# Optimization experiments

Measured on AMD Instinct MI355X. Metric: run time of the kernel, lower is better.

Reference implementation:

```python
import jax, jax.numpy as jnp
import numpy as np
import math

B, N, CS = 1, 2048, 384
H, C, PQK, PV = 12, 16, 4, 8
INF, EPS = 100000.0, 1e-08


def setup_inputs() -> dict:
    key = jax.random.key(0)
    ks = jax.random.split(key, 16)
    hc = H * C
    hpq = H * PQK * 3
    hpkv = H * (PQK + PV) * 3
    cod = H * (C + 4 * PV)
    sc = 0.02
    return {
        "s": jax.random.normal(ks[0], (B, N, CS), jnp.float32),
        "rot": jax.random.normal(ks[1], (B, N, 3, 3), jnp.float32),
        "trans": jax.random.normal(ks[2], (B, N, 3), jnp.float32),
        "mask": jnp.ones((B, N), jnp.float32),
        "Wq": jax.random.normal(ks[3], (hc, CS), jnp.float32) * sc,
        "bq": jnp.zeros((hc,), jnp.float32),
        "Wkv": jax.random.normal(ks[4], (2 * hc, CS), jnp.float32) * sc,
        "bkv": jnp.zeros((2 * hc,), jnp.float32),
        "Wqp": jax.random.normal(ks[5], (hpq, CS), jnp.float32) * sc,
        "bqp": jnp.zeros((hpq,), jnp.float32),
        "Wkvp": jax.random.normal(ks[6], (hpkv, CS), jnp.float32) * sc,
        "bkvp": jnp.zeros((hpkv,), jnp.float32),
        "head_weights": jnp.full((H,), 0.541324854612918, jnp.float32),
        "Wout": jax.random.normal(ks[7], (CS, H * cod // H), jnp.float32) * sc,
        "bout": jnp.zeros((CS,), jnp.float32),
    }


def _points(s, W, b, rot, trans, npts):
    # torch.split into 3 chunks of H*npts then stack at -1 -> [B,N,H*npts,3]
    p = jnp.einsum("bni,oi->bno", s, W) + b
    p = jnp.moveaxis(p.reshape(B, N, 3, H * npts), -2, -1)  # [B,N,H*npts,3]
    p = jnp.einsum("bnij,bnmj->bnmi", rot, p) + trans[:, :, None, :]  # rigid apply
    return p.reshape(B, N, H, npts, 3)


def reference(s, rot, trans, mask, Wq, bq, Wkv, bkv, Wqp, bqp, Wkvp, bkvp, head_weights, Wout, bout):
    q = (jnp.einsum("bni,oi->bno", s, Wq) + bq).reshape(B, N, H, C)
    kv = (jnp.einsum("bni,oi->bno", s, Wkv) + bkv).reshape(B, N, H, 2 * C)
    k, v = kv[..., :C], kv[..., C:]

    q_pts = _points(s, Wqp, bqp, rot, trans, PQK)             # [B,N,H,PQK,3]
    kv_pts = _points(s, Wkvp, bkvp, rot, trans, PQK + PV)
    k_pts, v_pts = kv_pts[..., :PQK, :], kv_pts[..., PQK:, :]  # [B,N,H,PQK,3], [B,N,H,PV,3]

    a = jnp.einsum("bihc,bjhc->bhij", q, k) * math.sqrt(1.0 / (3 * C))

    # sum_{p,c} |q_pts_i - k_pts_j|^2 via norm expansion (avoids [N,N,P,3])
    q2 = jnp.moveaxis(jnp.sum(q_pts ** 2, axis=(-1, -2)), -1, 1)  # [B,H,N]
    k2 = jnp.moveaxis(jnp.sum(k_pts ** 2, axis=(-1, -2)), -1, 1)
    cross = jnp.einsum("bihpc,bjhpc->bhij", q_pts, k_pts)
    d2 = q2[..., :, None] + k2[..., None, :] - 2.0 * cross       # [B,H,N,N]

    hw = jax.nn.softplus(head_weights) * math.sqrt(1.0 / (3 * (PQK * 9.0 / 2)))
    pt_att = -0.5 * hw[None, :, None, None] * d2

    sq_mask = INF * (mask[:, None, :, None] * mask[:, None, None, :] - 1.0)  # [B,1,N,N]
    a = jax.nn.softmax(a + pt_att + sq_mask, axis=-1)

    o = jnp.einsum("bhij,bjhc->bihc", a, v).reshape(B, N, H * C)
    o_pt = jnp.einsum("bhij,bjhpc->bihpc", a, v_pts)             # [B,N,H,PV,3]
    o_pt = jnp.einsum("bnji,bnhpj->bnhpi", rot, o_pt - trans[:, :, None, None, :])  # invert_apply

    dists = jnp.sqrt(jnp.sum(o_pt ** 2, axis=-1) + EPS).reshape(B, N, H * PV)
    o_pt_f = o_pt.reshape(B, N, H * PV, 3)
    feats = jnp.concatenate([o, o_pt_f[..., 0], o_pt_f[..., 1], o_pt_f[..., 2], dists], axis=-1)
    return jnp.einsum("bnf,of->bno", feats, Wout) + bout
```

## Files before the change

kernel.cpp:

```cpp
#include <hip/hip_runtime.h>
#include <hip/hip_bf16.h>
#include <cstdint>
#include <cstddef>

#define Hh    12
#define Nseq  2048
#define PSTR  1152
#define EPSm  1e-8f
#define MASKV 1024.0f

typedef unsigned short ushort_t;
typedef __attribute__((ext_vector_type(8))) short bf8_t;
typedef __attribute__((ext_vector_type(4))) short s4_t;
typedef __attribute__((ext_vector_type(4))) float f4_t;

#define OFF_PALL   0
#define OFF_WALLB  2359296
#define OFF_BALL   2580480
#define OFF_SB     2581632
#define OFF_WOUTB  2974848
#define OFF_FEATSB 3085440
#define OFF_AU     3675264
#define OFF_KU     4068480
#define OFF_VU     4461696
#define WS_FLOATS  5051520

__device__ __forceinline__ ushort_t bfr(float x) {
    union { float f; uint32_t u; } v; v.f = x;
    uint32_t r = v.u + 0x7FFFu + ((v.u >> 16) & 1u);
    return (ushort_t)(r >> 16);
}

__global__ __launch_bounds__(256) void prep(
    const float* __restrict__ s, const float* __restrict__ Wout,
    const float* __restrict__ Wq, const float* __restrict__ Wkv,
    const float* __restrict__ Wqp, const float* __restrict__ Wkvp,
    const float* __restrict__ bq, const float* __restrict__ bkv,
    const float* __restrict__ bqp, const float* __restrict__ bkvp,
    ushort_t* __restrict__ Wallb, float* __restrict__ ball,
    ushort_t* __restrict__ sb, ushort_t* __restrict__ Woutb)
{
    int idx = blockIdx.x * 256 + threadIdx.x;
    if (idx < 1152 * 384) {
        int r = idx / 384, c = idx % 384;
        float v;
        if (r < 192)      v = Wq [(size_t)r * 384 + c];
        else if (r < 576) v = Wkv[(size_t)(r - 192) * 384 + c];
        else if (r < 720) v = Wqp[(size_t)(r - 576) * 384 + c];
        else              v = Wkvp[(size_t)(r - 720) * 384 + c];
        Wallb[idx] = bfr(v);
    }
    if (idx < 1152) {
        float v;
        if (idx < 192)      v = bq[idx];
        else if (idx < 576) v = bkv[idx - 192];
        else if (idx < 720) v = bqp[idx - 576];
        else                v = bkvp[idx - 720];
        ball[idx] = v;
    }
    if (idx < 2048 * 384) sb[idx] = bfr(s[idx]);
    if (idx < 384 * 576)  Woutb[idx] = bfr(Wout[idx]);
}

template<int BM, int BN>
__global__ __launch_bounds__(256) void gemm_mfma(
    const ushort_t* __restrict__ A, const ushort_t* __restrict__ W,
    const float* __restrict__ bias, float* __restrict__ C,
    int M, int Nn, int K)
{
    constexpr int WM = BM / 2, WN = BN / 2;
    constexpr int MI = WM / 16, NJ = WN / 16;
    __shared__ ushort_t As[BM][40];
    __shared__ ushort_t Bs[BN][40];

    const int bm = blockIdx.y * BM;
    const int bn = blockIdx.x * BN;
    const int t  = threadIdx.x;
    const int w  = t >> 6, lane = t & 63;
    const int m  = lane & 15, quad = lane >> 4;
    const int wm = (w >> 1) * WM, wn = (w & 1) * WN;

    f4_t acc[MI][NJ];
    #pragma unroll
    for (int i2 = 0; i2 < MI; ++i2)
        #pragma unroll
        for (int j2 = 0; j2 < NJ; ++j2)
            acc[i2][j2] = (f4_t){0.f, 0.f, 0.f, 0.f};

    for (int k0 = 0; k0 < K; k0 += 32) {
        #pragma unroll
        for (int u = 0; u < BM / 64; ++u) {
            int e = t + u * 256;
            int r = e >> 2, kk = (e & 3) * 8;
            *(uint4*)&As[r][kk] = *(const uint4*)&A[(size_t)(bm + r) * K + k0 + kk];
        }
        #pragma unroll
        for (int u = 0; u < BN / 64; ++u) {
            int e = t + u * 256;
            int r = e >> 2, kk = (e & 3) * 8;
            *(uint4*)&Bs[r][kk] = *(const uint4*)&W[(size_t)(bn + r) * K + k0 + kk];
        }
        __syncthreads();
        bf8_t af[MI], bfv[NJ];
        #pragma unroll
        for (int x = 0; x < MI; ++x) af[x]  = *(const bf8_t*)&As[wm + x * 16 + m][quad * 8];
        #pragma unroll
        for (int x = 0; x < NJ; ++x) bfv[x] = *(const bf8_t*)&Bs[wn + x * 16 + m][quad * 8];
        #pragma unroll
        for (int i2 = 0; i2 < MI; ++i2)
            #pragma unroll
            for (int j2 = 0; j2 < NJ; ++j2)
                acc[i2][j2] = __builtin_amdgcn_mfma_f32_16x16x32_bf16(
                    af[i2], bfv[j2], acc[i2][j2], 0, 0, 0);
        __syncthreads();
    }

    #pragma unroll
    for (int j2 = 0; j2 < NJ; ++j2) {
        int col = bn + wn + j2 * 16 + m;
        float bb = bias[col];
        #pragma unroll
        for (int i2 = 0; i2 < MI; ++i2)
            #pragma unroll
            for (int r = 0; r < 4; ++r) {
                int row = bm + wm + i2 * 16 + quad * 4 + r;
                C[(size_t)row * Nn + col] = acc[i2][j2][r] + bb;
            }
    }
}

__global__ __launch_bounds__(128) void pack_aug(
    const float* __restrict__ Pall, const float* __restrict__ rot,
    const float* __restrict__ trans, const float* __restrict__ mask,
    const float* __restrict__ hwv,
    ushort_t* __restrict__ AU, ushort_t* __restrict__ KU,
    ushort_t* __restrict__ VU)
{
    __shared__ float S[8][1156];
    const int n0 = blockIdx.x * 8;
    const int t  = threadIdx.x;

    #pragma unroll
    for (int u = 0; u < 18; ++u) {
        int f = t + u * 128;
        int rr = f / 288, c4 = f % 288;
        float4 v = *(const float4*)&Pall[(size_t)(n0 + rr) * PSTR + c4 * 4];
        *(float4*)&S[rr][c4 * 4] = v;
    }
    __syncthreads();

    if (t >= 96) return;
    const int nl = t & 7, h = t >> 3;
    const int n  = n0 + nl;
    const float* row = S[nl];

    const float whw = 0.5f * logf(1.0f + expf(hwv[h])) * 0.13608276348795434f;
    const float scale_a = 0.14433756729740643f;

    float R[9], T[3];
    #pragma unroll
    for (int z = 0; z < 9; ++z) R[z] = rot[(size_t)n * 9 + z];
    #pragma unroll
    for (int d = 0; d < 3; ++d) T[d] = trans[(size_t)n * 3 + d];

    float qpv[12], q2 = 0.f;
    #pragma unroll
    for (int p = 0; p < 4; ++p) {
        float r0 = row[576 +   0 + h * 4 + p];
        float r1 = row[576 +  48 + h * 4 + p];
        float r2 = row[576 +  96 + h * 4 + p];
        #pragma unroll
        for (int d = 0; d < 3; ++d) {
            float o = R[d*3+0]*r0 + R[d*3+1]*r1 + R[d*3+2]*r2 + T[d];
            qpv[p * 3 + d] = o;
            q2 += o * o;
        }
    }

    float kpv[12], vpv[24], k2 = 0.f;
    #pragma unroll
    for (int pt = 0; pt < 12; ++pt) {
        float r0 = row[720 +   0 + h * 12 + pt];
        float r1 = row[720 + 144 + h * 12 + pt];
        float r2 = row[720 + 288 + h * 12 + pt];
        #pragma unroll
        for (int d = 0; d < 3; ++d) {
            float o = R[d*3+0]*r0 + R[d*3+1]*r1 + R[d*3+2]*r2 + T[d];
            if (pt < 4) { kpv[pt * 3 + d] = o; k2 += o * o; }
            else        { vpv[(pt - 4) * 3 + d] = o; }
        }
    }

    const float mi = mask[n];

    __align__(16) ushort_t a32[32];
    #pragma unroll
    for (int c = 0; c < 16; ++c) a32[c] = bfr(row[h * 16 + c] * scale_a);
    #pragma unroll
    for (int z = 0; z < 12; ++z) a32[16 + z] = bfr(qpv[z] * (2.0f * whw));
    a32[28] = bfr(-whw);
    a32[29] = bfr(-whw * q2);
    a32[30] = bfr(mi * MASKV);
    a32[31] = bfr(-MASKV);
    ushort_t* adst = AU + ((size_t)h * Nseq + n) * 32;
    #pragma unroll
    for (int u = 0; u < 4; ++u) ((uint4*)adst)[u] = ((const uint4*)a32)[u];

    const float* kvrow = row + 192 + h * 32;
    __align__(16) ushort_t k32[32];
    #pragma unroll
    for (int c = 0; c < 16; ++c) k32[c] = bfr(kvrow[c]);
    #pragma unroll
    for (int z = 0; z < 12; ++z) k32[16 + z] = bfr(kpv[z]);
    k32[28] = bfr(k2);
    k32[29] = 0x3F80;
    k32[30] = bfr(mi);
    k32[31] = 0x3F80;
    ushort_t* kdst = KU + ((size_t)h * Nseq + n) * 32;
    #pragma unroll
    for (int u = 0; u < 4; ++u) ((uint4*)kdst)[u] = ((const uint4*)k32)[u];

    ushort_t* vb = VU + (size_t)h * 98304 + (size_t)(n >> 5) * 1536 + (n & 31);
    #pragma unroll
    for (int c = 0; c < 16; ++c) vb[c * 32] = bfr(kvrow[16 + c]);
    #pragma unroll
    for (int z = 0; z < 24; ++z) vb[(16 + z) * 32] = bfr(vpv[z]);
    vb[40 * 32] = 0x3F80;
    #pragma unroll
    for (int c = 41; c < 48; ++c) vb[c * 32] = 0;
}

__device__ __forceinline__ bf8_t expack(f4_t s) {
    s4_t p;
    p[0] = (short)bfr(__expf(s[0]));
    p[1] = (short)bfr(__expf(s[1]));
    p[2] = (short)bfr(__expf(s[2]));
    p[3] = (short)bfr(__expf(s[3]));
    s4_t z = (s4_t)0;
    return __builtin_shufflevector(p, z, 0, 1, 2, 3, 4, 5, 6, 7);
}

__device__ __forceinline__ bf8_t vpad(s4_t v) {
    s4_t z = (s4_t)0;
    return __builtin_shufflevector(v, z, 0, 1, 2, 3, 4, 5, 6, 7);
}

struct KVTile { bf8_t kb0, kb1; s4_t v[6]; };

__device__ __forceinline__ KVTile load_tile(
    const ushort_t* __restrict__ kb_base, const ushort_t* __restrict__ vt,
    int m, int quad)
{
    KVTile tl;
    tl.kb0  = *(const bf8_t*)(kb_base);
    tl.kb1  = *(const bf8_t*)(kb_base + 16 * 32);
    tl.v[0] = *(const s4_t*)(vt +        m * 32 +      quad * 4);
    tl.v[1] = *(const s4_t*)(vt +  512 + m * 32 +      quad * 4);
    tl.v[2] = *(const s4_t*)(vt + 1024 + m * 32 +      quad * 4);
    tl.v[3] = *(const s4_t*)(vt +        m * 32 + 16 + quad * 4);
    tl.v[4] = *(const s4_t*)(vt +  512 + m * 32 + 16 + quad * 4);
    tl.v[5] = *(const s4_t*)(vt + 1024 + m * 32 + 16 + quad * 4);
    return tl;
}

__global__ __launch_bounds__(256, 3) void attn_mfma(
    const ushort_t* __restrict__ AU, const ushort_t* __restrict__ KU,
    const ushort_t* __restrict__ VU,
    const float* __restrict__ rot, const float* __restrict__ trans,
    ushort_t* __restrict__ featsb)
{
    __shared__ float red[4][32][49];

    const int b    = blockIdx.x;
    const int h    = b >> 6;
    const int ib   = b & 63;
    const int t    = threadIdx.x;
    const int w    = t >> 6;
    const int lane = t & 63;
    const int m    = lane & 15;
    const int quad = lane >> 4;
    const int i0   = ib * 32;

    bf8_t afA = *(const bf8_t*)(AU + ((size_t)h * Nseq + i0 +      m) * 32 + quad * 8);
    bf8_t afB = *(const bf8_t*)(AU + ((size_t)h * Nseq + i0 + 16 + m) * 32 + quad * 8);

    f4_t acc[6];
    #pragma unroll
    for (int z = 0; z < 6; ++z) acc[z] = (f4_t){0.f, 0.f, 0.f, 0.f};

    const int jb0 = w * 512;
    const ushort_t* kb_base = KU + ((size_t)h * Nseq + jb0 + m) * 32 + quad * 8;
    const ushort_t* v_base  = VU + (size_t)h * 98304 + (size_t)jb0 * 48;

    KVTile cur = load_tile(kb_base, v_base, m, quad);

    #pragma unroll
    for (int jt = 0; jt < 16; ++jt) {
        f4_t zz = (f4_t){0.f, 0.f, 0.f, 0.f};
        f4_t sXA = __builtin_amdgcn_mfma_f32_16x16x32_bf16(cur.kb0, afA, zz, 0, 0, 0);
        f4_t sXB = __builtin_amdgcn_mfma_f32_16x16x32_bf16(cur.kb0, afB, zz, 0, 0, 0);
        f4_t sYA = __builtin_amdgcn_mfma_f32_16x16x32_bf16(cur.kb1, afA, zz, 0, 0, 0);
        f4_t sYB = __builtin_amdgcn_mfma_f32_16x16x32_bf16(cur.kb1, afB, zz, 0, 0, 0);

        KVTile nxt;
        if (jt < 15)
            nxt = load_tile(kb_base + (size_t)(jt + 1) * 32 * 32,
                            v_base + (size_t)(jt + 1) * 1536, m, quad);

        bf8_t pXA = expack(sXA), pXB = expack(sXB);
        bf8_t pYA = expack(sYA), pYB = expack(sYB);
        bf8_t f0 = vpad(cur.v[0]), f1 = vpad(cur.v[1]), f2 = vpad(cur.v[2]);
        bf8_t g0 = vpad(cur.v[3]), g1 = vpad(cur.v[4]), g2 = vpad(cur.v[5]);

        acc[0] = __builtin_amdgcn_mfma_f32_16x16x32_bf16(pXA, f0, acc[0], 0, 0, 0);
        acc[0] = __builtin_amdgcn_mfma_f32_16x16x32_bf16(pYA, g0, acc[0], 0, 0, 0);
        acc[1] = __builtin_amdgcn_mfma_f32_16x16x32_bf16(pXA, f1, acc[1], 0, 0, 0);
        acc[1] = __builtin_amdgcn_mfma_f32_16x16x32_bf16(pYA, g1, acc[1], 0, 0, 0);
        acc[2] = __builtin_amdgcn_mfma_f32_16x16x32_bf16(pXA, f2, acc[2], 0, 0, 0);
        acc[2] = __builtin_amdgcn_mfma_f32_16x16x32_bf16(pYA, g2, acc[2], 0, 0, 0);
        acc[3] = __builtin_amdgcn_mfma_f32_16x16x32_bf16(pXB, f0, acc[3], 0, 0, 0);
        acc[3] = __builtin_amdgcn_mfma_f32_16x16x32_bf16(pYB, g0, acc[3], 0, 0, 0);
        acc[4] = __builtin_amdgcn_mfma_f32_16x16x32_bf16(pXB, f1, acc[4], 0, 0, 0);
        acc[4] = __builtin_amdgcn_mfma_f32_16x16x32_bf16(pYB, g1, acc[4], 0, 0, 0);
        acc[5] = __builtin_amdgcn_mfma_f32_16x16x32_bf16(pXB, f2, acc[5], 0, 0, 0);
        acc[5] = __builtin_amdgcn_mfma_f32_16x16x32_bf16(pYB, g2, acc[5], 0, 0, 0);

        cur = nxt;
    }

    #pragma unroll
    for (int r = 0; r < 4; ++r) {
        red[w][quad * 4 + r][m]           = acc[0][r];
        red[w][quad * 4 + r][16 + m]      = acc[1][r];
        red[w][quad * 4 + r][32 + m]      = acc[2][r];
        red[w][16 + quad * 4 + r][m]      = acc[3][r];
        red[w][16 + quad * 4 + r][16 + m] = acc[4][r];
        red[w][16 + quad * 4 + r][32 + m] = acc[5][r];
    }
    __syncthreads();

    #pragma unroll
    for (int u = 0; u < 6; ++u) {
        int e = t + u * 256;
        int rr = e / 48, cc = e % 48;
        red[0][rr][cc] = red[0][rr][cc] + red[1][rr][cc] + red[2][rr][cc] + red[3][rr][cc];
    }
    __syncthreads();

    if (t < 32) {
        const int i = i0 + t;
        float L   = red[0][t][40];
        float inv = 1.0f / L;
        float o[40];
        #pragma unroll
        for (int z = 0; z < 40; ++z) o[z] = red[0][t][z] * inv;

        ushort_t* f = featsb + (size_t)i * 576;
        #pragma unroll
        for (int c = 0; c < 16; ++c) f[h * 16 + c] = bfr(o[c]);

        float R[9], T[3];
        #pragma unroll
        for (int z = 0; z < 9; ++z) R[z] = rot[(size_t)i * 9 + z];
        #pragma unroll
        for (int d = 0; d < 3; ++d) T[d] = trans[(size_t)i * 3 + d];

        #pragma unroll
        for (int p8 = 0; p8 < 8; ++p8) {
            float g0 = o[16 + p8 * 3 + 0] - T[0];
            float g1 = o[16 + p8 * 3 + 1] - T[1];
            float g2 = o[16 + p8 * 3 + 2] - T[2];
            float xx = R[0] * g0 + R[3] * g1 + R[6] * g2;
            float yy = R[1] * g0 + R[4] * g1 + R[7] * g2;
            float zz = R[2] * g0 + R[5] * g1 + R[8] * g2;
            float dist = sqrtf(xx * xx + yy * yy + zz * zz + EPSm);
            f[192 + h * 8 + p8] = bfr(xx);
            f[288 + h * 8 + p8] = bfr(yy);
            f[384 + h * 8 + p8] = bfr(zz);
            f[480 + h * 8 + p8] = bfr(dist);
        }
    }
}

extern "C" void kernel_launch(void* const* d_in, const int* in_sizes, int n_in,
                              void* d_out, int out_size, void* d_ws, size_t ws_size,
                              hipStream_t stream)
{
    const float* s     = (const float*)d_in[0];
    const float* rot   = (const float*)d_in[1];
    const float* trans = (const float*)d_in[2];
    const float* mask  = (const float*)d_in[3];
    const float* Wq    = (const float*)d_in[4];
    const float* bq    = (const float*)d_in[5];
    const float* Wkv   = (const float*)d_in[6];
    const float* bkv   = (const float*)d_in[7];
    const float* Wqp   = (const float*)d_in[8];
    const float* bqp   = (const float*)d_in[9];
    const float* Wkvp  = (const float*)d_in[10];
    const float* bkvp  = (const float*)d_in[11];
    const float* hwv   = (const float*)d_in[12];
    const float* Wout  = (const float*)d_in[13];
    const float* bout  = (const float*)d_in[14];
    float* out = (float*)d_out;
    float* ws  = (float*)d_ws;

    if (ws_size < (size_t)WS_FLOATS * sizeof(float)) return;

    float*    Pall   = ws + OFF_PALL;
    ushort_t* Wallb  = (ushort_t*)(ws + OFF_WALLB);
    float*    ball   = ws + OFF_BALL;
    ushort_t* sb     = (ushort_t*)(ws + OFF_SB);
    ushort_t* Woutb  = (ushort_t*)(ws + OFF_WOUTB);
    ushort_t* featsb = (ushort_t*)(ws + OFF_FEATSB);
    ushort_t* AU     = (ushort_t*)(ws + OFF_AU);
    ushort_t* KU     = (ushort_t*)(ws + OFF_KU);
    ushort_t* VU     = (ushort_t*)(ws + OFF_VU);

    prep<<<dim3(3072), 256, 0, stream>>>(s, Wout, Wq, Wkv, Wqp, Wkvp,
                                         bq, bkv, bqp, bkvp,
                                         Wallb, ball, sb, Woutb);

    gemm_mfma<128, 64><<<dim3(1152 / 64, 2048 / 128), 256, 0, stream>>>(
        sb, Wallb, ball, Pall, 2048, 1152, 384);

    pack_aug<<<dim3(256), 128, 0, stream>>>(Pall, rot, trans, mask, hwv,
                                            AU, KU, VU);

    attn_mfma<<<dim3(768), 256, 0, stream>>>(AU, KU, VU, rot, trans, featsb);

    gemm_mfma<64, 64><<<dim3(384 / 64, 2048 / 64), 256, 0, stream>>>(
        featsb, Woutb, bout, out, 2048, 384, 576);
}
```

Before: 139.8 us.

## Fuse all stages into one persistent kernel with atomic grid barriers

Replaces the five separate launches (prep, projection GEMM, pack, attention, output GEMM) with one 768-block persistent kernel. Stages are separated by software grid barriers built on an atomic counter in the workspace, which is zeroed by a memset before launch. Shared memory becomes a union reused across stages. This removes launch gaps between kernels, but relies on all 768 blocks being co-resident (launch bounds of 3 blocks per CU) and leaves some blocks idle in the GEMM stages.

```diff
diff --git a/kernel.cpp b/kernel.cpp
--- a/kernel.cpp
+++ b/kernel.cpp
@@ -8,6 +8,7 @@
 #define PSTR  1152
 #define EPSm  1e-8f
 #define MASKV 1024.0f
+#define NBLK  768u
 
 typedef unsigned short ushort_t;
 typedef __attribute__((ext_vector_type(8))) short bf8_t;
@@ -23,7 +24,8 @@
 #define OFF_AU     3675264
 #define OFF_KU     4068480
 #define OFF_VU     4461696
-#define WS_FLOATS  5051520
+#define OFF_BAR    5051520
+#define WS_FLOATS  5051536
 
 __device__ __forceinline__ ushort_t bfr(float x) {
     union { float f; uint32_t u; } v; v.f = x;
@@ -31,203 +33,16 @@
     return (ushort_t)(r >> 16);
 }
 
-__global__ __launch_bounds__(256) void prep(
-    const float* __restrict__ s, const float* __restrict__ Wout,
-    const float* __restrict__ Wq, const float* __restrict__ Wkv,
-    const float* __restrict__ Wqp, const float* __restrict__ Wkvp,
-    const float* __restrict__ bq, const float* __restrict__ bkv,
-    const float* __restrict__ bqp, const float* __restrict__ bkvp,
-    ushort_t* __restrict__ Wallb, float* __restrict__ ball,
-    ushort_t* __restrict__ sb, ushort_t* __restrict__ Woutb)
-{
-    int idx = blockIdx.x * 256 + threadIdx.x;
-    if (idx < 1152 * 384) {
-        int r = idx / 384, c = idx % 384;
-        float v;
-        if (r < 192)      v = Wq [(size_t)r * 384 + c];
-        else if (r < 576) v = Wkv[(size_t)(r - 192) * 384 + c];
-        else if (r < 720) v = Wqp[(size_t)(r - 576) * 384 + c];
-        else              v = Wkvp[(size_t)(r - 720) * 384 + c];
-        Wallb[idx] = bfr(v);
-    }
-    if (idx < 1152) {
-        float v;
-        if (idx < 192)      v = bq[idx];
-        else if (idx < 576) v = bkv[idx - 192];
-        else if (idx < 720) v = bqp[idx - 576];
-        else                v = bkvp[idx - 720];
-        ball[idx] = v;
-    }
-    if (idx < 2048 * 384) sb[idx] = bfr(s[idx]);
-    if (idx < 384 * 576)  Woutb[idx] = bfr(Wout[idx]);
-}
-
-template<int BM, int BN>
-__global__ __launch_bounds__(256) void gemm_mfma(
-    const ushort_t* __restrict__ A, const ushort_t* __restrict__ W,
-    const float* __restrict__ bias, float* __restrict__ C,
-    int M, int Nn, int K)
-{
-    constexpr int WM = BM / 2, WN = BN / 2;
-    constexpr int MI = WM / 16, NJ = WN / 16;
-    __shared__ ushort_t As[BM][40];
-    __shared__ ushort_t Bs[BN][40];
-
-    const int bm = blockIdx.y * BM;
-    const int bn = blockIdx.x * BN;
-    const int t  = threadIdx.x;
-    const int w  = t >> 6, lane = t & 63;
-    const int m  = lane & 15, quad = lane >> 4;
-    const int wm = (w >> 1) * WM, wn = (w & 1) * WN;
-
-    f4_t acc[MI][NJ];
-    #pragma unroll
-    for (int i2 = 0; i2 < MI; ++i2)
-        #pragma unroll
-        for (int j2 = 0; j2 < NJ; ++j2)
-            acc[i2][j2] = (f4_t){0.f, 0.f, 0.f, 0.f};
-
-    for (int k0 = 0; k0 < K; k0 += 32) {
-        #pragma unroll
-        for (int u = 0; u < BM / 64; ++u) {
-            int e = t + u * 256;
-            int r = e >> 2, kk = (e & 3) * 8;
-            *(uint4*)&As[r][kk] = *(const uint4*)&A[(size_t)(bm + r) * K + k0 + kk];
-        }
-        #pragma unroll
-        for (int u = 0; u < BN / 64; ++u) {
-            int e = t + u * 256;
-            int r = e >> 2, kk = (e & 3) * 8;
-            *(uint4*)&Bs[r][kk] = *(const uint4*)&W[(size_t)(bn + r) * K + k0 + kk];
-        }
-        __syncthreads();
-        bf8_t af[MI], bfv[NJ];
-        #pragma unroll
-        for (int x = 0; x < MI; ++x) af[x]  = *(const bf8_t*)&As[wm + x * 16 + m][quad * 8];
-        #pragma unroll
-        for (int x = 0; x < NJ; ++x) bfv[x] = *(const bf8_t*)&Bs[wn + x * 16 + m][quad * 8];
-        #pragma unroll
-        for (int i2 = 0; i2 < MI; ++i2)
-            #pragma unroll
-            for (int j2 = 0; j2 < NJ; ++j2)
-                acc[i2][j2] = __builtin_amdgcn_mfma_f32_16x16x32_bf16(
-                    af[i2], bfv[j2], acc[i2][j2], 0, 0, 0);
-        __syncthreads();
-    }
-
-    #pragma unroll
-    for (int j2 = 0; j2 < NJ; ++j2) {
-        int col = bn + wn + j2 * 16 + m;
-        float bb = bias[col];
-        #pragma unroll
-        for (int i2 = 0; i2 < MI; ++i2)
-            #pragma unroll
-            for (int r = 0; r < 4; ++r) {
-                int row = bm + wm + i2 * 16 + quad * 4 + r;
-                C[(size_t)row * Nn + col] = acc[i2][j2][r] + bb;
-            }
-    }
-}
-
-__global__ __launch_bounds__(128) void pack_aug(
-    const float* __restrict__ Pall, const float* __restrict__ rot,
-    const float* __restrict__ trans, const float* __restrict__ mask,
-    const float* __restrict__ hwv,
-    ushort_t* __restrict__ AU, ushort_t* __restrict__ KU,
-    ushort_t* __restrict__ VU)
-{
-    __shared__ float S[8][1156];
-    const int n0 = blockIdx.x * 8;
-    const int t  = threadIdx.x;
-
-    #pragma unroll
-    for (int u = 0; u < 18; ++u) {
-        int f = t + u * 128;
-        int rr = f / 288, c4 = f % 288;
-        float4 v = *(const float4*)&Pall[(size_t)(n0 + rr) * PSTR + c4 * 4];
-        *(float4*)&S[rr][c4 * 4] = v;
-    }
+__device__ __forceinline__ void gridbar(unsigned* c) {
     __syncthreads();
-
-    if (t >= 96) return;
-    const int nl = t & 7, h = t >> 3;
-    const int n  = n0 + nl;
-    const float* row = S[nl];
-
-    const float whw = 0.5f * logf(1.0f + expf(hwv[h])) * 0.13608276348795434f;
-    const float scale_a = 0.14433756729740643f;
-
-    float R[9], T[3];
-    #pragma unroll
-    for (int z = 0; z < 9; ++z) R[z] = rot[(size_t)n * 9 + z];
-    #pragma unroll
-    for (int d = 0; d < 3; ++d) T[d] = trans[(size_t)n * 3 + d];
-
-    float qpv[12], q2 = 0.f;
-    #pragma unroll
-    for (int p = 0; p < 4; ++p) {
-        float r0 = row[576 +   0 + h * 4 + p];
-        float r1 = row[576 +  48 + h * 4 + p];
-        float r2 = row[576 +  96 + h * 4 + p];
-        #pragma unroll
-        for (int d = 0; d < 3; ++d) {
-            float o = R[d*3+0]*r0 + R[d*3+1]*r1 + R[d*3+2]*r2 + T[d];
-            qpv[p * 3 + d] = o;
-            q2 += o * o;
-        }
-    }
-
-    float kpv[12], vpv[24], k2 = 0.f;
-    #pragma unroll
-    for (int pt = 0; pt < 12; ++pt) {
-        float r0 = row[720 +   0 + h * 12 + pt];
-        float r1 = row[720 + 144 + h * 12 + pt];
-        float r2 = row[720 + 288 + h * 12 + pt];
-        #pragma unroll
-        for (int d = 0; d < 3; ++d) {
-            float o = R[d*3+0]*r0 + R[d*3+1]*r1 + R[d*3+2]*r2 + T[d];
-            if (pt < 4) { kpv[pt * 3 + d] = o; k2 += o * o; }
-            else        { vpv[(pt - 4) * 3 + d] = o; }
-        }
-    }
-
-    const float mi = mask[n];
-
-    __align__(16) ushort_t a32[32];
-    #pragma unroll
-    for (int c = 0; c < 16; ++c) a32[c] = bfr(row[h * 16 + c] * scale_a);
-    #pragma unroll
-    for (int z = 0; z < 12; ++z) a32[16 + z] = bfr(qpv[z] * (2.0f * whw));
-    a32[28] = bfr(-whw);
-    a32[29] = bfr(-whw * q2);
-    a32[30] = bfr(mi * MASKV);
-    a32[31] = bfr(-MASKV);
-    ushort_t* adst = AU + ((size_t)h * Nseq + n) * 32;
-    #pragma unroll
-    for (int u = 0; u < 4; ++u) ((uint4*)adst)[u] = ((const uint4*)a32)[u];
-
-    const float* kvrow = row + 192 + h * 32;
-    __align__(16) ushort_t k32[32];
-    #pragma unroll
-    for (int c = 0; c < 16; ++c) k32[c] = bfr(kvrow[c]);
-    #pragma unroll
-    for (int z = 0; z < 12; ++z) k32[16 + z] = bfr(kpv[z]);
-    k32[28] = bfr(k2);
-    k32[29] = 0x3F80;
-    k32[30] = bfr(mi);
-    k32[31] = 0x3F80;
-    ushort_t* kdst = KU + ((size_t)h * Nseq + n) * 32;
-    #pragma unroll
-    for (int u = 0; u < 4; ++u) ((uint4*)kdst)[u] = ((const uint4*)k32)[u];
-
-    ushort_t* vb = VU + (size_t)h * 98304 + (size_t)(n >> 5) * 1536 + (n & 31);
-    #pragma unroll
-    for (int c = 0; c < 16; ++c) vb[c * 32] = bfr(kvrow[16 + c]);
-    #pragma unroll
-    for (int z = 0; z < 24; ++z) vb[(16 + z) * 32] = bfr(vpv[z]);
-    vb[40 * 32] = 0x3F80;
-    #pragma unroll
-    for (int c = 41; c < 48; ++c) vb[c * 32] = 0;
+    if (threadIdx.x == 0) {
+        __threadfence();
+        __hip_atomic_fetch_add(c, 1u, __ATOMIC_ACQ_REL, __HIP_MEMORY_SCOPE_AGENT);
+        while (__hip_atomic_load(c, __ATOMIC_ACQUIRE, __HIP_MEMORY_SCOPE_AGENT) < NBLK)
+            __builtin_amdgcn_s_sleep(2);
+        __threadfence();
+    }
+    __syncthreads();
 }
 
 __device__ __forceinline__ bf8_t expack(f4_t s) {
@@ -263,123 +78,322 @@
     return tl;
 }
 
-__global__ __launch_bounds__(256, 3) void attn_mfma(
-    const ushort_t* __restrict__ AU, const ushort_t* __restrict__ KU,
-    const ushort_t* __restrict__ VU,
-    const float* __restrict__ rot, const float* __restrict__ trans,
-    ushort_t* __restrict__ featsb)
+union ShU {
+    struct { ushort_t As[64][40]; ushort_t Bs[64][40]; } g;
+    float S[8][1156];
+    float red[4][32][49];
+};
+
+__device__ __forceinline__ void gemm64(
+    int bx, int by, int t,
+    const ushort_t* __restrict__ A, const ushort_t* __restrict__ W,
+    const float* __restrict__ bias, float* __restrict__ C,
+    int Nn, int K, ShU& sh)
 {
-    __shared__ float red[4][32][49];
-
-    const int b    = blockIdx.x;
-    const int h    = b >> 6;
-    const int ib   = b & 63;
-    const int t    = threadIdx.x;
-    const int w    = t >> 6;
-    const int lane = t & 63;
-    const int m    = lane & 15;
-    const int quad = lane >> 4;
-    const int i0   = ib * 32;
-
-    bf8_t afA = *(const bf8_t*)(AU + ((size_t)h * Nseq + i0 +      m) * 32 + quad * 8);
-    bf8_t afB = *(const bf8_t*)(AU + ((size_t)h * Nseq + i0 + 16 + m) * 32 + quad * 8);
-
-    f4_t acc[6];
+    const int bm = by * 64, bn = bx * 64;
+    const int w = t >> 6, lane = t & 63;
+    const int m = lane & 15, quad = lane >> 4;
+    const int wm = (w >> 1) * 32, wn = (w & 1) * 32;
+
+    f4_t acc[2][2];
     #pragma unroll
-    for (int z = 0; z < 6; ++z) acc[z] = (f4_t){0.f, 0.f, 0.f, 0.f};
-
-    const int jb0 = w * 512;
-    const ushort_t* kb_base = KU + ((size_t)h * Nseq + jb0 + m) * 32 + quad * 8;
-    const ushort_t* v_base  = VU + (size_t)h * 98304 + (size_t)jb0 * 48;
-
-    KVTile cur = load_tile(kb_base, v_base, m, quad);
+    for (int i2 = 0; i2 < 2; ++i2)
+        #pragma unroll
+        for (int j2 = 0; j2 < 2; ++j2)
+            acc[i2][j2] = (f4_t){0.f, 0.f, 0.f, 0.f};
+
+    for (int k0 = 0; k0 < K; k0 += 32) {
+        {
+            int r = t >> 2, kk = (t & 3) * 8;
+            *(uint4*)&sh.g.As[r][kk] = *(const uint4*)&A[(size_t)(bm + r) * K + k0 + kk];
+            *(uint4*)&sh.g.Bs[r][kk] = *(const uint4*)&W[(size_t)(bn + r) * K + k0 + kk];
+        }
+        __syncthreads();
+        bf8_t af[2], bfv[2];
+        #pragma unroll
+        for (int x = 0; x < 2; ++x) {
+            af[x]  = *(const bf8_t*)&sh.g.As[wm + x * 16 + m][quad * 8];
+            bfv[x] = *(const bf8_t*)&sh.g.Bs[wn + x * 16 + m][quad * 8];
+        }
+        #pragma unroll
+        for (int i2 = 0; i2 < 2; ++i2)
+            #pragma unroll
+            for (int j2 = 0; j2 < 2; ++j2)
+                acc[i2][j2] = __builtin_amdgcn_mfma_f32_16x16x32_bf16(
+                    af[i2], bfv[j2], acc[i2][j2], 0, 0, 0);
+        __syncthreads();
+    }
 
     #pragma unroll
-    for (int jt = 0; jt < 16; ++jt) {
-        f4_t zz = (f4_t){0.f, 0.f, 0.f, 0.f};
-        f4_t sXA = __builtin_amdgcn_mfma_f32_16x16x32_bf16(cur.kb0, afA, zz, 0, 0, 0);
-        f4_t sXB = __builtin_amdgcn_mfma_f32_16x16x32_bf16(cur.kb0, afB, zz, 0, 0, 0);
-        f4_t sYA = __builtin_amdgcn_mfma_f32_16x16x32_bf16(cur.kb1, afA, zz, 0, 0, 0);
-        f4_t sYB = __builtin_amdgcn_mfma_f32_16x16x32_bf16(cur.kb1, afB, zz, 0, 0, 0);
-
-        KVTile nxt;
-        if (jt < 15)
-            nxt = load_tile(kb_base + (size_t)(jt + 1) * 32 * 32,
-                            v_base + (size_t)(jt + 1) * 1536, m, quad);
-
-        bf8_t pXA = expack(sXA), pXB = expack(sXB);
-        bf8_t pYA = expack(sYA), pYB = expack(sYB);
-        bf8_t f0 = vpad(cur.v[0]), f1 = vpad(cur.v[1]), f2 = vpad(cur.v[2]);
-        bf8_t g0 = vpad(cur.v[3]), g1 = vpad(cur.v[4]), g2 = vpad(cur.v[5]);
-
-        acc[0] = __builtin_amdgcn_mfma_f32_16x16x32_bf16(pXA, f0, acc[0], 0, 0, 0);
-        acc[0] = __builtin_amdgcn_mfma_f32_16x16x32_bf16(pYA, g0, acc[0], 0, 0, 0);
-        acc[1] = __builtin_amdgcn_mfma_f32_16x16x32_bf16(pXA, f1, acc[1], 0, 0, 0);
-        acc[1] = __builtin_amdgcn_mfma_f32_16x16x32_bf16(pYA, g1, acc[1], 0, 0, 0);
-        acc[2] = __builtin_amdgcn_mfma_f32_16x16x32_bf16(pXA, f2, acc[2], 0, 0, 0);
-        acc[2] = __builtin_amdgcn_mfma_f32_16x16x32_bf16(pYA, g2, acc[2], 0, 0, 0);
-        acc[3] = __builtin_amdgcn_mfma_f32_16x16x32_bf16(pXB, f0, acc[3], 0, 0, 0);
-        acc[3] = __builtin_amdgcn_mfma_f32_16x16x32_bf16(pYB, g0, acc[3], 0, 0, 0);
-        acc[4] = __builtin_amdgcn_mfma_f32_16x16x32_bf16(pXB, f1, acc[4], 0, 0, 0);
-        acc[4] = __builtin_amdgcn_mfma_f32_16x16x32_bf16(pYB, g1, acc[4], 0, 0, 0);
-        acc[5] = __builtin_amdgcn_mfma_f32_16x16x32_bf16(pXB, f2, acc[5], 0, 0, 0);
-        acc[5] = __builtin_amdgcn_mfma_f32_16x16x32_bf16(pYB, g2, acc[5], 0, 0, 0);
-
-        cur = nxt;
-    }
-
-    #pragma unroll
-    for (int r = 0; r < 4; ++r) {
-        red[w][quad * 4 + r][m]           = acc[0][r];
-        red[w][quad * 4 + r][16 + m]      = acc[1][r];
-        red[w][quad * 4 + r][32 + m]      = acc[2][r];
-        red[w][16 + quad * 4 + r][m]      = acc[3][r];
-        red[w][16 + quad * 4 + r][16 + m] = acc[4][r];
-        red[w][16 + quad * 4 + r][32 + m] = acc[5][r];
-    }
-    __syncthreads();
-
-    #pragma unroll
-    for (int u = 0; u < 6; ++u) {
-        int e = t + u * 256;
-        int rr = e / 48, cc = e % 48;
-        red[0][rr][cc] = red[0][rr][cc] + red[1][rr][cc] + red[2][rr][cc] + red[3][rr][cc];
-    }
-    __syncthreads();
-
-    if (t < 32) {
-        const int i = i0 + t;
-        float L   = red[0][t][40];
-        float inv = 1.0f / L;
-        float o[40];
-        #pragma unroll
-        for (int z = 0; z < 40; ++z) o[z] = red[0][t][z] * inv;
-
-        ushort_t* f = featsb + (size_t)i * 576;
-        #pragma unroll
-        for (int c = 0; c < 16; ++c) f[h * 16 + c] = bfr(o[c]);
-
-        float R[9], T[3];
-        #pragma unroll
-        for (int z = 0; z < 9; ++z) R[z] = rot[(size_t)i * 9 + z];
-        #pragma unroll
-        for (int d = 0; d < 3; ++d) T[d] = trans[(size_t)i * 3 + d];
-
-        #pragma unroll
-        for (int p8 = 0; p8 < 8; ++p8) {
-            float g0 = o[16 + p8 * 3 + 0] - T[0];
-            float g1 = o[16 + p8 * 3 + 1] - T[1];
-            float g2 = o[16 + p8 * 3 + 2] - T[2];
-            float xx = R[0] * g0 + R[3] * g1 + R[6] * g2;
-            float yy = R[1] * g0 + R[4] * g1 + R[7] * g2;
-            float zz = R[2] * g0 + R[5] * g1 + R[8] * g2;
-            float dist = sqrtf(xx * xx + yy * yy + zz * zz + EPSm);
-            f[192 + h * 8 + p8] = bfr(xx);
-            f[288 + h * 8 + p8] = bfr(yy);
-            f[384 + h * 8 + p8] = bfr(zz);
-            f[480 + h * 8 + p8] = bfr(dist);
-        }
-    }
+    for (int j2 = 0; j2 < 2; ++j2) {
+        int col = bn + wn + j2 * 16 + m;
+        float bb = bias[col];
+        #pragma unroll
+        for (int i2 = 0; i2 < 2; ++i2)
+            #pragma unroll
+            for (int r = 0; r < 4; ++r) {
+                int row = bm + wm + i2 * 16 + quad * 4 + r;
+                C[(size_t)row * Nn + col] = acc[i2][j2][r] + bb;
+            }
+    }
+}
+
+__global__ __launch_bounds__(256, 3) void mega(
+    const float* __restrict__ s, const float* __restrict__ rot,
+    const float* __restrict__ trans, const float* __restrict__ mask,
+    const float* __restrict__ Wq, const float* __restrict__ bq,
+    const float* __restrict__ Wkv, const float* __restrict__ bkv,
+    const float* __restrict__ Wqp, const float* __restrict__ bqp,
+    const float* __restrict__ Wkvp, const float* __restrict__ bkvp,
+    const float* __restrict__ hwv, const float* __restrict__ Wout,
+    const float* __restrict__ bout,
+    float* __restrict__ Pall, ushort_t* __restrict__ Wallb,
+    float* __restrict__ ball, ushort_t* __restrict__ sb,
+    ushort_t* __restrict__ Woutb, ushort_t* __restrict__ featsb,
+    ushort_t* __restrict__ AU, ushort_t* __restrict__ KU,
+    ushort_t* __restrict__ VU, unsigned* __restrict__ bar,
+    float* __restrict__ out)
+{
+    __shared__ ShU sh;
+    const int bid = blockIdx.x;
+    const int t   = threadIdx.x;
+    const int base = bid * 256 + t;
+
+    for (int idx = base; idx < 2048 * 384; idx += 768 * 256)
+        sb[idx] = bfr(s[idx]);
+    for (int idx = base; idx < 1152 * 384; idx += 768 * 256) {
+        int r = idx / 384, c = idx % 384;
+        float v;
+        if (r < 192)      v = Wq [(size_t)r * 384 + c];
+        else if (r < 576) v = Wkv[(size_t)(r - 192) * 384 + c];
+        else if (r < 720) v = Wqp[(size_t)(r - 576) * 384 + c];
+        else              v = Wkvp[(size_t)(r - 720) * 384 + c];
+        Wallb[idx] = bfr(v);
+    }
+    for (int idx = base; idx < 384 * 576; idx += 768 * 256)
+        Woutb[idx] = bfr(Wout[idx]);
+    if (base < 1152) {
+        float v;
+        if (base < 192)      v = bq[base];
+        else if (base < 576) v = bkv[base - 192];
+        else if (base < 720) v = bqp[base - 576];
+        else                 v = bkvp[base - 720];
+        ball[base] = v;
+    }
+    gridbar(bar + 0);
+
+    if (bid < 576)
+        gemm64(bid % 18, bid / 18, t, sb, Wallb, ball, Pall, PSTR, 384, sh);
+    gridbar(bar + 1);
+
+    if (bid < 256) {
+        const int n0 = bid * 8;
+        #pragma unroll
+        for (int u = 0; u < 9; ++u) {
+            int f = t + u * 256;
+            int rr = f / 288, c4 = f % 288;
+            float4 v = *(const float4*)&Pall[(size_t)(n0 + rr) * PSTR + c4 * 4];
+            *(float4*)&sh.S[rr][c4 * 4] = v;
+        }
+        __syncthreads();
+
+        if (t < 96) {
+            const int nl = t & 7, h = t >> 3;
+            const int n  = n0 + nl;
+            const float* row = sh.S[nl];
+
+            const float whw = 0.5f * logf(1.0f + expf(hwv[h])) * 0.13608276348795434f;
+            const float scale_a = 0.14433756729740643f;
+
+            float R[9], T[3];
+            #pragma unroll
+            for (int z = 0; z < 9; ++z) R[z] = rot[(size_t)n * 9 + z];
+            #pragma unroll
+            for (int d = 0; d < 3; ++d) T[d] = trans[(size_t)n * 3 + d];
+
+            float qpv[12], q2 = 0.f;
+            #pragma unroll
+            for (int p = 0; p < 4; ++p) {
+                float r0 = row[576 +   0 + h * 4 + p];
+                float r1 = row[576 +  48 + h * 4 + p];
+                float r2 = row[576 +  96 + h * 4 + p];
+                #pragma unroll
+                for (int d = 0; d < 3; ++d) {
+                    float o = R[d*3+0]*r0 + R[d*3+1]*r1 + R[d*3+2]*r2 + T[d];
+                    qpv[p * 3 + d] = o;
+                    q2 += o * o;
+                }
+            }
+
+            float kpv[12], vpv[24], k2 = 0.f;
+            #pragma unroll
+            for (int pt = 0; pt < 12; ++pt) {
+                float r0 = row[720 +   0 + h * 12 + pt];
+                float r1 = row[720 + 144 + h * 12 + pt];
+                float r2 = row[720 + 288 + h * 12 + pt];
+                #pragma unroll
+                for (int d = 0; d < 3; ++d) {
+                    float o = R[d*3+0]*r0 + R[d*3+1]*r1 + R[d*3+2]*r2 + T[d];
+                    if (pt < 4) { kpv[pt * 3 + d] = o; k2 += o * o; }
+                    else        { vpv[(pt - 4) * 3 + d] = o; }
+                }
+            }
+
+            const float mi = mask[n];
+
+            __align__(16) ushort_t a32[32];
+            #pragma unroll
+            for (int c = 0; c < 16; ++c) a32[c] = bfr(row[h * 16 + c] * scale_a);
+            #pragma unroll
+            for (int z = 0; z < 12; ++z) a32[16 + z] = bfr(qpv[z] * (2.0f * whw));
+            a32[28] = bfr(-whw);
+            a32[29] = bfr(-whw * q2);
+            a32[30] = bfr(mi * MASKV);
+            a32[31] = bfr(-MASKV);
+            ushort_t* adst = AU + ((size_t)h * Nseq + n) * 32;
+            #pragma unroll
+            for (int u = 0; u < 4; ++u) ((uint4*)adst)[u] = ((const uint4*)a32)[u];
+
+            const float* kvrow = row + 192 + h * 32;
+            __align__(16) ushort_t k32[32];
+            #pragma unroll
+            for (int c = 0; c < 16; ++c) k32[c] = bfr(kvrow[c]);
+            #pragma unroll
+            for (int z = 0; z < 12; ++z) k32[16 + z] = bfr(kpv[z]);
+            k32[28] = bfr(k2);
+            k32[29] = 0x3F80;
+            k32[30] = bfr(mi);
+            k32[31] = 0x3F80;
+            ushort_t* kdst = KU + ((size_t)h * Nseq + n) * 32;
+            #pragma unroll
+            for (int u = 0; u < 4; ++u) ((uint4*)kdst)[u] = ((const uint4*)k32)[u];
+
+            ushort_t* vb = VU + (size_t)h * 98304 + (size_t)(n >> 5) * 1536 + (n & 31);
+            #pragma unroll
+            for (int c = 0; c < 16; ++c) vb[c * 32] = bfr(kvrow[16 + c]);
+            #pragma unroll
+            for (int z = 0; z < 24; ++z) vb[(16 + z) * 32] = bfr(vpv[z]);
+            vb[40 * 32] = 0x3F80;
+            #pragma unroll
+            for (int c = 41; c < 48; ++c) vb[c * 32] = 0;
+        }
+    }
+    gridbar(bar + 2);
+
+    {
+        const int h    = bid >> 6;
+        const int ib   = bid & 63;
+        const int w    = t >> 6;
+        const int lane = t & 63;
+        const int m    = lane & 15;
+        const int quad = lane >> 4;
+        const int i0   = ib * 32;
+
+        bf8_t afA = *(const bf8_t*)(AU + ((size_t)h * Nseq + i0 +      m) * 32 + quad * 8);
+        bf8_t afB = *(const bf8_t*)(AU + ((size_t)h * Nseq + i0 + 16 + m) * 32 + quad * 8);
+
+        f4_t acc[6];
+        #pragma unroll
+        for (int z = 0; z < 6; ++z) acc[z] = (f4_t){0.f, 0.f, 0.f, 0.f};
+
+        const int jb0 = w * 512;
+        const ushort_t* kb_base = KU + ((size_t)h * Nseq + jb0 + m) * 32 + quad * 8;
+        const ushort_t* v_base  = VU + (size_t)h * 98304 + (size_t)jb0 * 48;
+
+        KVTile cur = load_tile(kb_base, v_base, m, quad);
+
+        #pragma unroll
+        for (int jt = 0; jt < 16; ++jt) {
+            f4_t zz = (f4_t){0.f, 0.f, 0.f, 0.f};
+            f4_t sXA = __builtin_amdgcn_mfma_f32_16x16x32_bf16(cur.kb0, afA, zz, 0, 0, 0);
+            f4_t sXB = __builtin_amdgcn_mfma_f32_16x16x32_bf16(cur.kb0, afB, zz, 0, 0, 0);
+            f4_t sYA = __builtin_amdgcn_mfma_f32_16x16x32_bf16(cur.kb1, afA, zz, 0, 0, 0);
+            f4_t sYB = __builtin_amdgcn_mfma_f32_16x16x32_bf16(cur.kb1, afB, zz, 0, 0, 0);
+
+            KVTile nxt;
+            if (jt < 15)
+                nxt = load_tile(kb_base + (size_t)(jt + 1) * 1024,
+                                v_base + (size_t)(jt + 1) * 1536, m, quad);
+
+            bf8_t pXA = expack(sXA), pXB = expack(sXB);
+            bf8_t pYA = expack(sYA), pYB = expack(sYB);
+            bf8_t f0 = vpad(cur.v[0]), f1 = vpad(cur.v[1]), f2 = vpad(cur.v[2]);
+            bf8_t g0 = vpad(cur.v[3]), g1 = vpad(cur.v[4]), g2 = vpad(cur.v[5]);
+
+            acc[0] = __builtin_amdgcn_mfma_f32_16x16x32_bf16(pXA, f0, acc[0], 0, 0, 0);
+            acc[0] = __builtin_amdgcn_mfma_f32_16x16x32_bf16(pYA, g0, acc[0], 0, 0, 0);
+            acc[1] = __builtin_amdgcn_mfma_f32_16x16x32_bf16(pXA, f1, acc[1], 0, 0, 0);
+            acc[1] = __builtin_amdgcn_mfma_f32_16x16x32_bf16(pYA, g1, acc[1], 0, 0, 0);
+            acc[2] = __builtin_amdgcn_mfma_f32_16x16x32_bf16(pXA, f2, acc[2], 0, 0, 0);
+            acc[2] = __builtin_amdgcn_mfma_f32_16x16x32_bf16(pYA, g2, acc[2], 0, 0, 0);
+            acc[3] = __builtin_amdgcn_mfma_f32_16x16x32_bf16(pXB, f0, acc[3], 0, 0, 0);
+            acc[3] = __builtin_amdgcn_mfma_f32_16x16x32_bf16(pYB, g0, acc[3], 0, 0, 0);
+            acc[4] = __builtin_amdgcn_mfma_f32_16x16x32_bf16(pXB, f1, acc[4], 0, 0, 0);
+            acc[4] = __builtin_amdgcn_mfma_f32_16x16x32_bf16(pYB, g1, acc[4], 0, 0, 0);
+            acc[5] = __builtin_amdgcn_mfma_f32_16x16x32_bf16(pXB, f2, acc[5], 0, 0, 0);
+            acc[5] = __builtin_amdgcn_mfma_f32_16x16x32_bf16(pYB, g2, acc[5], 0, 0, 0);
+
+            cur = nxt;
+        }
+
+        #pragma unroll
+        for (int r = 0; r < 4; ++r) {
+            sh.red[w][quad * 4 + r][m]           = acc[0][r];
+            sh.red[w][quad * 4 + r][16 + m]      = acc[1][r];
+            sh.red[w][quad * 4 + r][32 + m]      = acc[2][r];
+            sh.red[w][16 + quad * 4 + r][m]      = acc[3][r];
+            sh.red[w][16 + quad * 4 + r][16 + m] = acc[4][r];
+            sh.red[w][16 + quad * 4 + r][32 + m] = acc[5][r];
+        }
+        __syncthreads();
+
+        #pragma unroll
+        for (int u = 0; u < 6; ++u) {
+            int e = t + u * 256;
+            int rr = e / 48, cc = e % 48;
+            sh.red[0][rr][cc] = sh.red[0][rr][cc] + sh.red[1][rr][cc]
+                              + sh.red[2][rr][cc] + sh.red[3][rr][cc];
+        }
+        __syncthreads();
+
+        if (t < 32) {
+            const int i = i0 + t;
+            float L   = sh.red[0][t][40];
+            float inv = 1.0f / L;
+            float o[40];
+            #pragma unroll
+            for (int z = 0; z < 40; ++z) o[z] = sh.red[0][t][z] * inv;
+
+            ushort_t* f = featsb + (size_t)i * 576;
+            #pragma unroll
+            for (int c = 0; c < 16; ++c) f[h * 16 + c] = bfr(o[c]);
+
+            float R[9], T[3];
+            #pragma unroll
+            for (int z = 0; z < 9; ++z) R[z] = rot[(size_t)i * 9 + z];
+            #pragma unroll
+            for (int d = 0; d < 3; ++d) T[d] = trans[(size_t)i * 3 + d];
+
+            #pragma unroll
+            for (int p8 = 0; p8 < 8; ++p8) {
+                float g0 = o[16 + p8 * 3 + 0] - T[0];
+                float g1 = o[16 + p8 * 3 + 1] - T[1];
+                float g2 = o[16 + p8 * 3 + 2] - T[2];
+                float xx = R[0] * g0 + R[3] * g1 + R[6] * g2;
+                float yy = R[1] * g0 + R[4] * g1 + R[7] * g2;
+                float zz = R[2] * g0 + R[5] * g1 + R[8] * g2;
+                float dist = sqrtf(xx * xx + yy * yy + zz * zz + EPSm);
+                f[192 + h * 8 + p8] = bfr(xx);
+                f[288 + h * 8 + p8] = bfr(yy);
+                f[384 + h * 8 + p8] = bfr(zz);
+                f[480 + h * 8 + p8] = bfr(dist);
+            }
+        }
+    }
+    gridbar(bar + 3);
+
+    if (bid < 192)
+        gemm64(bid % 6, bid / 6, t, featsb, Woutb, bout, out, 384, 576, sh);
 }
 
 extern "C" void kernel_launch(void* const* d_in, const int* in_sizes, int n_in,
@@ -415,19 +429,12 @@
     ushort_t* AU     = (ushort_t*)(ws + OFF_AU);
     ushort_t* KU     = (ushort_t*)(ws + OFF_KU);
     ushort_t* VU     = (ushort_t*)(ws + OFF_VU);
-
-    prep<<<dim3(3072), 256, 0, stream>>>(s, Wout, Wq, Wkv, Wqp, Wkvp,
-                                         bq, bkv, bqp, bkvp,
-                                         Wallb, ball, sb, Woutb);
-
-    gemm_mfma<128, 64><<<dim3(1152 / 64, 2048 / 128), 256, 0, stream>>>(
-        sb, Wallb, ball, Pall, 2048, 1152, 384);
-
-    pack_aug<<<dim3(256), 128, 0, stream>>>(Pall, rot, trans, mask, hwv,
-                                            AU, KU, VU);
-
-    attn_mfma<<<dim3(768), 256, 0, stream>>>(AU, KU, VU, rot, trans, featsb);
-
-    gemm_mfma<64, 64><<<dim3(384 / 64, 2048 / 64), 256, 0, stream>>>(
-        featsb, Woutb, bout, out, 2048, 384, 576);
-}
+    unsigned* bar    = (unsigned*)(ws + OFF_BAR);
+
+    hipMemsetAsync(bar, 0, 4 * sizeof(unsigned), stream);
+
+    mega<<<dim3(NBLK), 256, 0, stream>>>(
+        s, rot, trans, mask, Wq, bq, Wkv, bkv, Wqp, bqp, Wkvp, bkvp,
+        hwv, Wout, bout,
+        Pall, Wallb, ball, sb, Woutb, featsb, AU, KU, VU, bar, out);
+}
```

Result: slower. 552.2 us (+295.0%).
